# Kernel optimization log

Measured on AMD Instinct MI355X. Metric: run time of the kernel, lower is better.

## Reference

```python
import jax, jax.numpy as jnp
import numpy as np

NUM_HEADS = 16
NEG_INF = -1e18


def setup_inputs() -> dict:
    key = jax.random.key(0)
    ks = jax.random.split(key, 9)
    T, B, D = 2048, 2, 1024
    s = 1.0 / np.sqrt(D)
    return {
        "query": jax.random.normal(ks[0], (T, B, D), jnp.float32),
        "q_w": jax.random.normal(ks[1], (D, D), jnp.float32) * s,
        "q_b": jax.random.normal(ks[2], (D,), jnp.float32) * 0.02,
        "k_w": jax.random.normal(ks[3], (D, D), jnp.float32) * s,
        "k_b": jax.random.normal(ks[4], (D,), jnp.float32) * 0.02,
        "v_w": jax.random.normal(ks[5], (D, D), jnp.float32) * s,
        "v_b": jax.random.normal(ks[6], (D,), jnp.float32) * 0.02,
        "out_w": jax.random.normal(ks[7], (D, D), jnp.float32) * s,
        "out_b": jax.random.normal(ks[8], (D,), jnp.float32) * 0.02,
    }


def reference(query, q_w, q_b, k_w, k_b, v_w, v_b, out_w, out_b):
    # query: [T, B, D] (Time x Batch x Channel). Self-attention, causal mask,
    # dropout=0, need_weights=True.
    T, B, D = query.shape
    H = NUM_HEADS
    hd = D // H
    scaling = 1.0 / jnp.sqrt(jnp.asarray(hd, query.dtype))

    q = (query @ q_w.T + q_b) * scaling
    k = query @ k_w.T + k_b
    v = query @ v_w.T + v_b

    def split_heads(x):  # [T, B, D] -> [B, H, T, hd]
        return x.reshape(T, B, H, hd).transpose(1, 2, 0, 3)

    qh, kh, vh = split_heads(q), split_heads(k), split_heads(v)

    # scores: [B, H, T, T]
    scores = jnp.einsum("bhtd,bhsd->bhts", qh, kh)
    causal = jnp.triu(jnp.full((T, T), NEG_INF, dtype=scores.dtype), k=1)
    scores = scores + causal

    probs = jax.nn.softmax(scores, axis=-1)
    attn = jnp.einsum("bhts,bhsd->bhtd", probs, vh)  # [B, H, T, hd]
    attn = attn.transpose(2, 0, 1, 3).reshape(T, B, D)
    out = attn @ out_w.T + out_b

    # averaged attention weights over heads: [B, T, T]
    avg_weights = probs.sum(axis=1) / H
    return out, avg_weights
```

## Files before the change

kernel.cpp:

```cpp
#include <hip/hip_runtime.h>
#include <hip/hip_bf16.h>
#include <stdint.h>

typedef __hip_bfloat16 bf16;
using short8 = __attribute__((ext_vector_type(8))) short;
using f32x4  = __attribute__((ext_vector_type(4))) float;

#define TDIM 2048
#define BDIM 2
#define DDIM 1024
#define HNUM 16
#define HD   64
#define MDIM 4096
#define M0   16.0f

__device__ __forceinline__ f32x4 mfma16(short8 a, short8 b, f32x4 c) {
  return __builtin_amdgcn_mfma_f32_16x16x32_bf16(a, b, c, 0, 0, 0);
}

union S8 { short8 v; bf16 h[8]; };
union P4 { uint2 u; bf16 h[4]; };

__global__ __launch_bounds__(256) void cast_all_kernel(
    const float* __restrict__ q, const float* __restrict__ wq,
    const float* __restrict__ wk, const float* __restrict__ wv,
    const float* __restrict__ wo, bf16* __restrict__ dst) {
  int t4 = blockIdx.x * blockDim.x + threadIdx.x;
  int idx = t4 * 4;
  const float* s;
  if (idx < 4194304)      s = q  + idx;
  else if (idx < 5242880) s = wq + (idx - 4194304);
  else if (idx < 6291456) s = wk + (idx - 5242880);
  else if (idx < 7340032) s = wv + (idx - 6291456);
  else                    s = wo + (idx - 7340032);
  float4 v = *(const float4*)s;
  union { ushort4 u; bf16 b[4]; } pk;
  pk.b[0] = __float2bfloat16(v.x);
  pk.b[1] = __float2bfloat16(v.y);
  pk.b[2] = __float2bfloat16(v.z);
  pk.b[3] = __float2bfloat16(v.w);
  *(ushort4*)(dst + idx) = pk.u;
}

__global__ __launch_bounds__(256) void qkv_kernel(
    const bf16* __restrict__ X, const bf16* __restrict__ Wq,
    const bf16* __restrict__ Wk, const bf16* __restrict__ Wv,
    const float* __restrict__ qb, const float* __restrict__ kb,
    const float* __restrict__ vb, bf16* __restrict__ Qo,
    bf16* __restrict__ Ko, bf16* __restrict__ Vto) {
  __shared__ __align__(16) bf16 Xs[64][72];
  __shared__ __align__(16) bf16 Qs[64][72];
  __shared__ __align__(16) bf16 Ks[64][72];
  __shared__ __align__(16) bf16 Vs[64][72];
  const int tid  = threadIdx.x;
  const int lane = tid & 63, wave = tid >> 6;
  const int m0 = blockIdx.y * 64, n0 = blockIdx.x * 64;
  const int wm = (wave >> 1) * 32, wn = (wave & 1) * 32;
  const int fr = lane & 15, quad = lane >> 4, q8 = quad * 8;
  const int r = tid >> 3, cc = (tid & 7) * 8;
  f32x4 aq[2][2] = {}, ak[2][2] = {}, av[2][2] = {};
  const bf16* xp0 = X  + (size_t)(m0 + r) * DDIM + cc;
  const bf16* xp1 = xp0 + 32 * DDIM;
  const bf16* qp0 = Wq + (size_t)(n0 + r) * DDIM + cc;
  const bf16* qp1 = qp0 + 32 * DDIM;
  const bf16* kp0 = Wk + (size_t)(n0 + r) * DDIM + cc;
  const bf16* kp1 = kp0 + 32 * DDIM;
  const bf16* vp0 = Wv + (size_t)(n0 + r) * DDIM + cc;
  const bf16* vp1 = vp0 + 32 * DDIM;
  for (int k0 = 0; k0 < DDIM; k0 += 64) {
    uint4 xv0 = *(const uint4*)(xp0 + k0), xv1 = *(const uint4*)(xp1 + k0);
    uint4 qv0 = *(const uint4*)(qp0 + k0), qv1 = *(const uint4*)(qp1 + k0);
    uint4 kv0 = *(const uint4*)(kp0 + k0), kv1 = *(const uint4*)(kp1 + k0);
    uint4 vv0 = *(const uint4*)(vp0 + k0), vv1 = *(const uint4*)(vp1 + k0);
    __syncthreads();
    *(uint4*)&Xs[r][cc] = xv0; *(uint4*)&Xs[r + 32][cc] = xv1;
    *(uint4*)&Qs[r][cc] = qv0; *(uint4*)&Qs[r + 32][cc] = qv1;
    *(uint4*)&Ks[r][cc] = kv0; *(uint4*)&Ks[r + 32][cc] = kv1;
    *(uint4*)&Vs[r][cc] = vv0; *(uint4*)&Vs[r + 32][cc] = vv1;
    __syncthreads();
#pragma unroll
    for (int kk = 0; kk < 2; kk++) {
      const int ko = kk * 32 + q8;
      short8 xf[2], qf[2], kf[2], vf[2];
#pragma unroll
      for (int j = 0; j < 2; j++) {
        xf[j] = *(const short8*)&Xs[wm + j * 16 + fr][ko];
        qf[j] = *(const short8*)&Qs[wn + j * 16 + fr][ko];
        kf[j] = *(const short8*)&Ks[wn + j * 16 + fr][ko];
        vf[j] = *(const short8*)&Vs[wn + j * 16 + fr][ko];
      }
#pragma unroll
      for (int i = 0; i < 2; i++)
#pragma unroll
        for (int j = 0; j < 2; j++) {
          aq[i][j] = mfma16(xf[i], qf[j], aq[i][j]);
          ak[i][j] = mfma16(xf[i], kf[j], ak[i][j]);
          av[i][j] = mfma16(vf[i], xf[j], av[i][j]);
        }
    }
  }
#pragma unroll
  for (int mt = 0; mt < 2; mt++)
#pragma unroll
    for (int nt = 0; nt < 2; nt++)
#pragma unroll
      for (int i = 0; i < 4; i++) {
        {
          int gm = m0 + wm + mt * 16 + quad * 4 + i;
          int gn = n0 + wn + nt * 16 + fr;
          int t = gm >> 1, bb = gm & 1, h = gn >> 6, e = gn & 63;
          size_t o = ((size_t)(bb * HNUM + h) * TDIM + t) * HD + e;
          Qo[o] = __float2bfloat16((aq[mt][nt][i] + qb[gn]) * 0.125f);
          Ko[o] = __float2bfloat16(ak[mt][nt][i] + kb[gn]);
        }
        {
          int gf = n0 + wn + mt * 16 + quad * 4 + i;
          int gt = m0 + wm + nt * 16 + fr;
          int t = gt >> 1, bb = gt & 1, h = gf >> 6, e = gf & 63;
          Vto[((size_t)(bb * HNUM + h) * HD + e) * TDIM + t] =
              __float2bfloat16(av[mt][nt][i] + vb[gf]);
        }
      }
}

__global__ __launch_bounds__(256) void gemm_out_kernel(
    const bf16* __restrict__ P0, const bf16* __restrict__ P1,
    const bf16* __restrict__ Bw, const float* __restrict__ l0buf,
    const float* __restrict__ l1buf, const float* __restrict__ bias,
    float* __restrict__ of32) {
  __shared__ __align__(16) bf16 As[64][40];
  __shared__ __align__(16) bf16 Bs[64][40];
  __shared__ float sInv[64][16];
  const int tid  = threadIdx.x;
  const int lane = tid & 63, wave = tid >> 6;
  const int m0 = blockIdx.y * 64, n0 = blockIdx.x * 64;
  const int wm = (wave >> 1) * 32, wn = (wave & 1) * 32;
  const int fr = lane & 15, quad = lane >> 4, q8 = quad * 8;
  const int ldr = tid >> 2, ldc = (tid & 3) * 8;
#pragma unroll
  for (int e = 0; e < 4; e++) {
    int idx = tid * 4 + e;
    int row = idx >> 4, h = idx & 15;
    int gm = m0 + row, t = gm >> 1, bb = gm & 1;
    size_t li = (size_t)(bb * HNUM + h) * TDIM + t;
    sInv[row][h] = 1.0f / (l0buf[li] + l1buf[li]);
  }
  __syncthreads();
  f32x4 acc[2][2] = {};
  const size_t arow = (size_t)(m0 + ldr) * DDIM + ldc;
  const bf16* bptr = Bw + (size_t)(n0 + ldr) * DDIM + ldc;
  for (int k0 = 0; k0 < DDIM; k0 += 32) {
    S8 a0, a1, apk;
    a0.v = *(const short8*)&P0[arow + k0];
    a1.v = *(const short8*)&P1[arow + k0];
    uint4 bvv = *(const uint4*)(bptr + k0);
    float inv = sInv[ldr][k0 >> 6];
#pragma unroll
    for (int k = 0; k < 8; k++)
      apk.h[k] = __float2bfloat16(
          (__bfloat162float(a0.h[k]) + __bfloat162float(a1.h[k])) * inv);
    __syncthreads();
    *(short8*)&As[ldr][ldc] = apk.v;
    *(uint4*)&Bs[ldr][ldc] = bvv;
    __syncthreads();
    short8 af[2], bfr[2];
    af[0]  = *(const short8*)&As[wm + fr][q8];
    af[1]  = *(const short8*)&As[wm + 16 + fr][q8];
    bfr[0] = *(const short8*)&Bs[wn + fr][q8];
    bfr[1] = *(const short8*)&Bs[wn + 16 + fr][q8];
    acc[0][0] = mfma16(af[0], bfr[0], acc[0][0]);
    acc[0][1] = mfma16(af[0], bfr[1], acc[0][1]);
    acc[1][0] = mfma16(af[1], bfr[0], acc[1][0]);
    acc[1][1] = mfma16(af[1], bfr[1], acc[1][1]);
  }
#pragma unroll
  for (int mt = 0; mt < 2; mt++)
#pragma unroll
    for (int nt = 0; nt < 2; nt++)
#pragma unroll
      for (int i = 0; i < 4; i++) {
        int gm = m0 + wm + mt * 16 + quad * 4 + i;
        int gn = n0 + wn + nt * 16 + fr;
        of32[(size_t)gm * DDIM + gn] = acc[mt][nt][i] + bias[gn];
      }
}

__global__ __launch_bounds__(256) void attn_split_kernel(
    const bf16* __restrict__ Q, const bf16* __restrict__ K,
    const bf16* __restrict__ Vt, bf16* __restrict__ P0o,
    bf16* __restrict__ P1o, float* __restrict__ l0buf,
    float* __restrict__ l1buf) {
  __shared__ __align__(16) bf16 Ks[2][64][40];
  __shared__ __align__(16) bf16 Vs[2][64][40];
  __shared__ __align__(16) bf16 pt[4][32][72];
  const int tid = threadIdx.x, lane = tid & 63, wave = tid >> 6;
  const int bid = blockIdx.x;
  const int part = bid & 1, bh = (bid >> 1) & 31, t128 = 15 - (bid >> 6);
  const int b = bh >> 4, h = bh & 15;
  const int t0 = t128 * 128 + wave * 32;
  const int fr = lane & 15, quad = lane >> 4, q8 = quad * 8;
  const bf16* Qp = Q + ((size_t)bh * TDIM + t0) * HD;
  const bf16* Kp = K + (size_t)bh * TDIM * HD;
  const bf16* Vp = Vt + (size_t)bh * HD * TDIM;
  short8 aq[2][2];
  aq[0][0] = *(const short8*)&Qp[fr * HD + q8];
  aq[0][1] = *(const short8*)&Qp[fr * HD + 32 + q8];
  aq[1][0] = *(const short8*)&Qp[(16 + fr) * HD + q8];
  aq[1][1] = *(const short8*)&Qp[(16 + fr) * HD + 32 + q8];
  const int Cb = 2 * t128 + 2, C0 = t128 + 1;
  const int clo = part ? C0 : 0, chi = part ? Cb : C0;
  const int sr0 = tid >> 3, scc = (tid & 7) * 8, sr1 = sr0 + 32;
  const int ssub = scc >> 5, scol = scc & 31;
  f32x4 oacc[2][4] = {};
  float lsum[2] = {0.f, 0.f};
  uint4 kv0, kv1, vv0, vv1;
  auto ldglob = [&](int c) {
    int s0 = c * 64;
    kv0 = *(const uint4*)&Kp[(size_t)(s0 + sr0) * HD + scc];
    kv1 = *(const uint4*)&Kp[(size_t)(s0 + sr1) * HD + scc];
    vv0 = *(const uint4*)&Vp[(size_t)sr0 * TDIM + s0 + scc];
    vv1 = *(const uint4*)&Vp[(size_t)sr1 * TDIM + s0 + scc];
  };
  ldglob(clo);
  for (int c = clo; c < chi; c++) {
    __syncthreads();
    *(uint4*)&Ks[ssub][sr0][scol] = kv0;
    *(uint4*)&Ks[ssub][sr1][scol] = kv1;
    *(uint4*)&Vs[ssub][sr0][scol] = vv0;
    *(uint4*)&Vs[ssub][sr1][scol] = vv1;
    __syncthreads();
    if (c + 1 < chi) ldglob(c + 1);
    const int s0 = c * 64;
    f32x4 scT[2][4] = {};
#pragma unroll
    for (int j = 0; j < 4; j++) {
      short8 k0f = *(const short8*)&Ks[0][j * 16 + fr][q8];
      short8 k1f = *(const short8*)&Ks[1][j * 16 + fr][q8];
      scT[0][j] = mfma16(k0f, aq[0][0], scT[0][j]);
      scT[0][j] = mfma16(k1f, aq[0][1], scT[0][j]);
      scT[1][j] = mfma16(k0f, aq[1][0], scT[1][j]);
      scT[1][j] = mfma16(k1f, aq[1][1], scT[1][j]);
    }
#pragma unroll
    for (int g = 0; g < 2; g++) {
      const int t_row = t0 + g * 16 + fr;
#pragma unroll
      for (int j = 0; j < 4; j++) {
        const int s_base = s0 + j * 16 + quad * 4;
        P4 pk;
#pragma unroll
        for (int i = 0; i < 4; i++) {
          float p = 0.f;
          if (s_base + i <= t_row) {
            p = __expf(scT[g][j][i] - M0);
            lsum[g] += p;
          }
          pk.h[i] = __float2bfloat16(p);
        }
        *(uint2*)&pt[wave][g * 16 + fr][j * 16 + quad * 4] = pk.u;
      }
    }
#pragma unroll
    for (int c2 = 0; c2 < 2; c2++) {
      short8 ap0 = *(const short8*)&pt[wave][fr][c2 * 32 + q8];
      short8 ap1 = *(const short8*)&pt[wave][16 + fr][c2 * 32 + q8];
#pragma unroll
      for (int nt = 0; nt < 4; nt++) {
        short8 vf = *(const short8*)&Vs[c2][nt * 16 + fr][q8];
        oacc[0][nt] = mfma16(ap0, vf, oacc[0][nt]);
        oacc[1][nt] = mfma16(ap1, vf, oacc[1][nt]);
      }
    }
  }
  float lr[2];
#pragma unroll
  for (int g = 0; g < 2; g++) {
    float l = lsum[g];
    l += __shfl_xor(l, 16);
    l += __shfl_xor(l, 32);
    lr[g] = l;
  }
  bf16*  Op = part ? P1o : P0o;
  float* lb = part ? l1buf : l0buf;
#pragma unroll
  for (int g = 0; g < 2; g++)
#pragma unroll
    for (int nt = 0; nt < 4; nt++)
#pragma unroll
      for (int i = 0; i < 4; i++) {
        int t_row = t0 + g * 16 + quad * 4 + i;
        int col = h * HD + nt * 16 + fr;
        Op[((size_t)t_row * BDIM + b) * DDIM + col] =
            __float2bfloat16(oacc[g][nt][i]);
      }
  if (quad == 0) {
    lb[(size_t)bh * TDIM + t0 + fr]      = lr[0];
    lb[(size_t)bh * TDIM + t0 + 16 + fr] = lr[1];
  }
}

__global__ __launch_bounds__(256) void avg_kernel(
    const bf16* __restrict__ Q, const bf16* __restrict__ K,
    const float* __restrict__ l0buf, const float* __restrict__ l1buf,
    float* __restrict__ avgw) {
  const int tid = threadIdx.x;
  int r = blockIdx.x;
  const int b = (r >= 2048) ? 1 : 0;
  r &= 2047;
  float* avp = avgw + (size_t)b * TDIM * TDIM;
  if (r >= 1056) {
    int r2 = r - 1056;
    int ti = 0;
    while (ti < 31 && (ti + 1) * (62 - ti) <= r2) ti++;
    int si = (2 * ti + 2) + (r2 - ti * (63 - ti));
    int t0b = ti * 64, s0 = si * 32;
#pragma unroll
    for (int k = 0; k < 2; k++) {
      int off = (tid * 2 + k) * 4;
      *(float4*)&avp[(size_t)(t0b + (off >> 5)) * TDIM + s0 + (off & 31)] =
          make_float4(0.f, 0.f, 0.f, 0.f);
    }
    return;
  }
  int ti = 0;
  while ((ti + 1) * (ti + 2) <= r) ti++;
  const int si = r - ti * (ti + 1);
  const int t0b = ti * 64, s0 = si * 32;

  __shared__ __align__(16) bf16 Qs[2][64][40];
  __shared__ __align__(16) bf16 Ks2[2][32][40];
  __shared__ float sinvl[HNUM][64];
#pragma unroll
  for (int k = 0; k < 4; k++) {
    int idx = tid + k * 256;
    size_t li = (size_t)(b * HNUM + (idx >> 6)) * TDIM + t0b + (idx & 63);
    sinvl[idx >> 6][idx & 63] = 1.0f / (l0buf[li] + l1buf[li]);
  }
  const int lane = tid & 63, wave = tid >> 6;
  const int fr = lane & 15, quad = lane >> 4, q8 = quad * 8;
  const int twr = wave * 16;
  const int qr0 = tid >> 3, qcc = (tid & 7) * 8, qr1 = qr0 + 32;
  const int qsub = qcc >> 5, qcol = qcc & 31;
  const bf16* Qb = Q + (size_t)b * HNUM * TDIM * HD;
  const bf16* Kb = K + (size_t)b * HNUM * TDIM * HD;
  uint4 qv0, qv1, kv1;
  auto ldh = [&](int hh) {
    const bf16* Qh = Qb + (size_t)hh * TDIM * HD;
    const bf16* Kh = Kb + (size_t)hh * TDIM * HD;
    qv0 = *(const uint4*)&Qh[(size_t)(t0b + qr0) * HD + qcc];
    qv1 = *(const uint4*)&Qh[(size_t)(t0b + qr1) * HD + qcc];
    kv1 = *(const uint4*)&Kh[(size_t)(s0 + (qr0 & 31)) * HD + qcc];
  };
  ldh(0);
  f32x4 facc[2] = {};
  for (int hh = 0; hh < HNUM; hh++) {
    __syncthreads();
    *(uint4*)&Qs[qsub][qr0][qcol] = qv0;
    *(uint4*)&Qs[qsub][qr1][qcol] = qv1;
    if (qr0 < 32) *(uint4*)&Ks2[qsub][qr0][qcol] = kv1;
    else          *(uint4*)&Ks2[qsub][qr0 - 32][qcol] = kv1;
    __syncthreads();
    if (hh + 1 < HNUM) ldh(hh + 1);
    short8 a0 = *(const short8*)&Qs[0][twr + fr][q8];
    short8 a1 = *(const short8*)&Qs[1][twr + fr][q8];
#pragma unroll
    for (int nt = 0; nt < 2; nt++) {
      short8 b0 = *(const short8*)&Ks2[0][nt * 16 + fr][q8];
      short8 b1 = *(const short8*)&Ks2[1][nt * 16 + fr][q8];
      f32x4 sc = {};
      sc = mfma16(a0, b0, sc);
      sc = mfma16(a1, b1, sc);
#pragma unroll
      for (int i = 0; i < 4; i++) {
        int tr = twr + quad * 4 + i;
        if (s0 + nt * 16 + fr <= t0b + tr)
          facc[nt][i] += __expf(sc[i] - M0) * sinvl[hh][tr];
      }
    }
  }
#pragma unroll
  for (int nt = 0; nt < 2; nt++)
#pragma unroll
    for (int i = 0; i < 4; i++)
      avp[(size_t)(t0b + twr + quad * 4 + i) * TDIM + s0 + nt * 16 + fr] =
          facc[nt][i] * 0.0625f;
}

extern "C" void kernel_launch(void* const* d_in, const int* in_sizes, int n_in,
                              void* d_out, int out_size, void* d_ws, size_t ws_size,
                              hipStream_t stream) {
  const float* q   = (const float*)d_in[0];
  const float* q_w = (const float*)d_in[1];
  const float* q_b = (const float*)d_in[2];
  const float* k_w = (const float*)d_in[3];
  const float* k_b = (const float*)d_in[4];
  const float* v_w = (const float*)d_in[5];
  const float* v_b = (const float*)d_in[6];
  const float* o_w = (const float*)d_in[7];
  const float* o_b = (const float*)d_in[8];
  float* out = (float*)d_out;
  float* avg = out + (size_t)MDIM * DDIM;

  bf16* ws  = (bf16*)d_ws;
  bf16* Xbf = ws;
  bf16* Wq  = ws + 4194304;
  bf16* Wk  = ws + 5242880;
  bf16* Wv  = ws + 6291456;
  bf16* Wo  = ws + 7340032;
  bf16* Qw  = ws + 8388608;
  bf16* Kw  = ws + 12582912;
  bf16* Vt  = ws + 16777216;
  bf16* P1  = ws + 20971520;
  bf16* P0  = ws;
  float* l0 = (float*)(ws + 4194304);
  float* l1 = (float*)(ws + 4325376);

  cast_all_kernel<<<8192, 256, 0, stream>>>(q, q_w, k_w, v_w, o_w, Xbf);
  qkv_kernel<<<dim3(16, 64), 256, 0, stream>>>(Xbf, Wq, Wk, Wv, q_b, k_b, v_b,
                                               Qw, Kw, Vt);
  attn_split_kernel<<<1024, 256, 0, stream>>>(Qw, Kw, Vt, P0, P1, l0, l1);
  avg_kernel<<<4096, 256, 0, stream>>>(Qw, Kw, l0, l1, avg);
  gemm_out_kernel<<<dim3(16, 64), 256, 0, stream>>>(P0, P1, Wo, l0, l1, o_b, out);
}
```

Measured before the change: 252.0 us.

## Enlarge QKV tile to 128 rows and prefetch next k-tile in projection GEMMs

The QKV projection kernel now computes a 128x64 output tile per block instead of 64x64, so each loaded weight tile is reused across twice as many rows and the grid is halved. Both the QKV and output GEMMs now load the next k-slice into registers while the current slice is being multiplied, a register-level software pipeline meant to hide global memory latency. The output GEMM's k-step also grows from 32 to 64 to cut barrier count. The cost is more registers and LDS per block, which may lower occupancy, and fewer blocks in the QKV grid.

```diff
diff --git a/kernel.cpp b/kernel.cpp
--- a/kernel.cpp
+++ b/kernel.cpp
@@ -42,84 +42,99 @@
   *(ushort4*)(dst + idx) = pk.u;
 }
 
-__global__ __launch_bounds__(256) void qkv_kernel(
+__global__ __launch_bounds__(256, 2) void qkv_kernel(
     const bf16* __restrict__ X, const bf16* __restrict__ Wq,
     const bf16* __restrict__ Wk, const bf16* __restrict__ Wv,
     const float* __restrict__ qb, const float* __restrict__ kb,
     const float* __restrict__ vb, bf16* __restrict__ Qo,
     bf16* __restrict__ Ko, bf16* __restrict__ Vto) {
-  __shared__ __align__(16) bf16 Xs[64][72];
+  __shared__ __align__(16) bf16 Xs[128][72];
   __shared__ __align__(16) bf16 Qs[64][72];
   __shared__ __align__(16) bf16 Ks[64][72];
   __shared__ __align__(16) bf16 Vs[64][72];
   const int tid  = threadIdx.x;
   const int lane = tid & 63, wave = tid >> 6;
-  const int m0 = blockIdx.y * 64, n0 = blockIdx.x * 64;
-  const int wm = (wave >> 1) * 32, wn = (wave & 1) * 32;
+  const int m0 = blockIdx.y * 128, n0 = blockIdx.x * 64;
+  const int wm = (wave >> 1) * 64, wn = (wave & 1) * 32;
   const int fr = lane & 15, quad = lane >> 4, q8 = quad * 8;
   const int r = tid >> 3, cc = (tid & 7) * 8;
-  f32x4 aq[2][2] = {}, ak[2][2] = {}, av[2][2] = {};
-  const bf16* xp0 = X  + (size_t)(m0 + r) * DDIM + cc;
-  const bf16* xp1 = xp0 + 32 * DDIM;
-  const bf16* qp0 = Wq + (size_t)(n0 + r) * DDIM + cc;
-  const bf16* qp1 = qp0 + 32 * DDIM;
-  const bf16* kp0 = Wk + (size_t)(n0 + r) * DDIM + cc;
-  const bf16* kp1 = kp0 + 32 * DDIM;
-  const bf16* vp0 = Wv + (size_t)(n0 + r) * DDIM + cc;
-  const bf16* vp1 = vp0 + 32 * DDIM;
+  f32x4 aq[4][2] = {}, ak[4][2] = {}, av[2][4] = {};
+  const bf16* xp = X  + (size_t)(m0 + r) * DDIM + cc;
+  const bf16* qp = Wq + (size_t)(n0 + r) * DDIM + cc;
+  const bf16* kp = Wk + (size_t)(n0 + r) * DDIM + cc;
+  const bf16* vp = Wv + (size_t)(n0 + r) * DDIM + cc;
+  uint4 xv[4], qv[2], kv[2], vv[2];
+  auto ld = [&](int k0) {
+#pragma unroll
+    for (int j = 0; j < 4; j++)
+      xv[j] = *(const uint4*)(xp + (size_t)j * 32 * DDIM + k0);
+#pragma unroll
+    for (int j = 0; j < 2; j++) {
+      qv[j] = *(const uint4*)(qp + (size_t)j * 32 * DDIM + k0);
+      kv[j] = *(const uint4*)(kp + (size_t)j * 32 * DDIM + k0);
+      vv[j] = *(const uint4*)(vp + (size_t)j * 32 * DDIM + k0);
+    }
+  };
+  ld(0);
   for (int k0 = 0; k0 < DDIM; k0 += 64) {
-    uint4 xv0 = *(const uint4*)(xp0 + k0), xv1 = *(const uint4*)(xp1 + k0);
-    uint4 qv0 = *(const uint4*)(qp0 + k0), qv1 = *(const uint4*)(qp1 + k0);
-    uint4 kv0 = *(const uint4*)(kp0 + k0), kv1 = *(const uint4*)(kp1 + k0);
-    uint4 vv0 = *(const uint4*)(vp0 + k0), vv1 = *(const uint4*)(vp1 + k0);
-    __syncthreads();
-    *(uint4*)&Xs[r][cc] = xv0; *(uint4*)&Xs[r + 32][cc] = xv1;
-    *(uint4*)&Qs[r][cc] = qv0; *(uint4*)&Qs[r + 32][cc] = qv1;
-    *(uint4*)&Ks[r][cc] = kv0; *(uint4*)&Ks[r + 32][cc] = kv1;
-    *(uint4*)&Vs[r][cc] = vv0; *(uint4*)&Vs[r + 32][cc] = vv1;
-    __syncthreads();
+    __syncthreads();
+#pragma unroll
+    for (int j = 0; j < 4; j++) *(uint4*)&Xs[r + j * 32][cc] = xv[j];
+#pragma unroll
+    for (int j = 0; j < 2; j++) {
+      *(uint4*)&Qs[r + j * 32][cc] = qv[j];
+      *(uint4*)&Ks[r + j * 32][cc] = kv[j];
+      *(uint4*)&Vs[r + j * 32][cc] = vv[j];
+    }
+    __syncthreads();
+    if (k0 + 64 < DDIM) ld(k0 + 64);
 #pragma unroll
     for (int kk = 0; kk < 2; kk++) {
       const int ko = kk * 32 + q8;
-      short8 xf[2], qf[2], kf[2], vf[2];
+      short8 xf[4], qf[2], kf[2], vf[2];
+#pragma unroll
+      for (int i = 0; i < 4; i++)
+        xf[i] = *(const short8*)&Xs[wm + i * 16 + fr][ko];
 #pragma unroll
       for (int j = 0; j < 2; j++) {
-        xf[j] = *(const short8*)&Xs[wm + j * 16 + fr][ko];
         qf[j] = *(const short8*)&Qs[wn + j * 16 + fr][ko];
         kf[j] = *(const short8*)&Ks[wn + j * 16 + fr][ko];
         vf[j] = *(const short8*)&Vs[wn + j * 16 + fr][ko];
       }
 #pragma unroll
-      for (int i = 0; i < 2; i++)
+      for (int i = 0; i < 4; i++)
 #pragma unroll
         for (int j = 0; j < 2; j++) {
           aq[i][j] = mfma16(xf[i], qf[j], aq[i][j]);
           ak[i][j] = mfma16(xf[i], kf[j], ak[i][j]);
-          av[i][j] = mfma16(vf[i], xf[j], av[i][j]);
+          av[j][i] = mfma16(vf[j], xf[i], av[j][i]);
         }
     }
   }
 #pragma unroll
-  for (int mt = 0; mt < 2; mt++)
+  for (int mt = 0; mt < 4; mt++)
 #pragma unroll
     for (int nt = 0; nt < 2; nt++)
 #pragma unroll
       for (int i = 0; i < 4; i++) {
-        {
-          int gm = m0 + wm + mt * 16 + quad * 4 + i;
-          int gn = n0 + wn + nt * 16 + fr;
-          int t = gm >> 1, bb = gm & 1, h = gn >> 6, e = gn & 63;
-          size_t o = ((size_t)(bb * HNUM + h) * TDIM + t) * HD + e;
-          Qo[o] = __float2bfloat16((aq[mt][nt][i] + qb[gn]) * 0.125f);
-          Ko[o] = __float2bfloat16(ak[mt][nt][i] + kb[gn]);
-        }
-        {
-          int gf = n0 + wn + mt * 16 + quad * 4 + i;
-          int gt = m0 + wm + nt * 16 + fr;
-          int t = gt >> 1, bb = gt & 1, h = gf >> 6, e = gf & 63;
-          Vto[((size_t)(bb * HNUM + h) * HD + e) * TDIM + t] =
-              __float2bfloat16(av[mt][nt][i] + vb[gf]);
-        }
+        int gm = m0 + wm + mt * 16 + quad * 4 + i;
+        int gn = n0 + wn + nt * 16 + fr;
+        int t = gm >> 1, bb = gm & 1, h = gn >> 6, e = gn & 63;
+        size_t o = ((size_t)(bb * HNUM + h) * TDIM + t) * HD + e;
+        Qo[o] = __float2bfloat16((aq[mt][nt][i] + qb[gn]) * 0.125f);
+        Ko[o] = __float2bfloat16(ak[mt][nt][i] + kb[gn]);
+      }
+#pragma unroll
+  for (int vt = 0; vt < 2; vt++)
+#pragma unroll
+    for (int xt = 0; xt < 4; xt++)
+#pragma unroll
+      for (int i = 0; i < 4; i++) {
+        int gf = n0 + wn + vt * 16 + quad * 4 + i;
+        int gt = m0 + wm + xt * 16 + fr;
+        int t = gt >> 1, bb = gt & 1, h = gf >> 6, e = gf & 63;
+        Vto[((size_t)(bb * HNUM + h) * HD + e) * TDIM + t] =
+            __float2bfloat16(av[vt][xt][i] + vb[gf]);
       }
 }
 
@@ -128,15 +143,15 @@
     const bf16* __restrict__ Bw, const float* __restrict__ l0buf,
     const float* __restrict__ l1buf, const float* __restrict__ bias,
     float* __restrict__ of32) {
-  __shared__ __align__(16) bf16 As[64][40];
-  __shared__ __align__(16) bf16 Bs[64][40];
+  __shared__ __align__(16) bf16 As[64][72];
+  __shared__ __align__(16) bf16 Bs[64][72];
   __shared__ float sInv[64][16];
   const int tid  = threadIdx.x;
   const int lane = tid & 63, wave = tid >> 6;
   const int m0 = blockIdx.y * 64, n0 = blockIdx.x * 64;
   const int wm = (wave >> 1) * 32, wn = (wave & 1) * 32;
   const int fr = lane & 15, quad = lane >> 4, q8 = quad * 8;
-  const int ldr = tid >> 2, ldc = (tid & 3) * 8;
+  const int ldr = tid >> 3, ldc = (tid & 7) * 8;
 #pragma unroll
   for (int e = 0; e < 4; e++) {
     int idx = tid * 4 + e;
@@ -145,33 +160,54 @@
     size_t li = (size_t)(bb * HNUM + h) * TDIM + t;
     sInv[row][h] = 1.0f / (l0buf[li] + l1buf[li]);
   }
+  f32x4 acc[2][2] = {};
+  const size_t ar0 = (size_t)(m0 + ldr) * DDIM + ldc;
+  const size_t ar1 = ar0 + (size_t)32 * DDIM;
+  const bf16* bp0 = Bw + (size_t)(n0 + ldr) * DDIM + ldc;
+  const bf16* bp1 = bp0 + (size_t)32 * DDIM;
+  S8 p00, p10, p01, p11;
+  uint4 bv0, bv1;
+  auto ld = [&](int k0) {
+    p00.v = *(const short8*)&P0[ar0 + k0];
+    p10.v = *(const short8*)&P1[ar0 + k0];
+    p01.v = *(const short8*)&P0[ar1 + k0];
+    p11.v = *(const short8*)&P1[ar1 + k0];
+    bv0 = *(const uint4*)(bp0 + k0);
+    bv1 = *(const uint4*)(bp1 + k0);
+  };
+  ld(0);
   __syncthreads();
-  f32x4 acc[2][2] = {};
-  const size_t arow = (size_t)(m0 + ldr) * DDIM + ldc;
-  const bf16* bptr = Bw + (size_t)(n0 + ldr) * DDIM + ldc;
-  for (int k0 = 0; k0 < DDIM; k0 += 32) {
-    S8 a0, a1, apk;
-    a0.v = *(const short8*)&P0[arow + k0];
-    a1.v = *(const short8*)&P1[arow + k0];
-    uint4 bvv = *(const uint4*)(bptr + k0);
-    float inv = sInv[ldr][k0 >> 6];
-#pragma unroll
-    for (int k = 0; k < 8; k++)
-      apk.h[k] = __float2bfloat16(
-          (__bfloat162float(a0.h[k]) + __bfloat162float(a1.h[k])) * inv);
-    __syncthreads();
-    *(short8*)&As[ldr][ldc] = apk.v;
-    *(uint4*)&Bs[ldr][ldc] = bvv;
-    __syncthreads();
-    short8 af[2], bfr[2];
-    af[0]  = *(const short8*)&As[wm + fr][q8];
-    af[1]  = *(const short8*)&As[wm + 16 + fr][q8];
-    bfr[0] = *(const short8*)&Bs[wn + fr][q8];
-    bfr[1] = *(const short8*)&Bs[wn + 16 + fr][q8];
-    acc[0][0] = mfma16(af[0], bfr[0], acc[0][0]);
-    acc[0][1] = mfma16(af[0], bfr[1], acc[0][1]);
-    acc[1][0] = mfma16(af[1], bfr[0], acc[1][0]);
-    acc[1][1] = mfma16(af[1], bfr[1], acc[1][1]);
+  for (int k0 = 0; k0 < DDIM; k0 += 64) {
+    const float inv0 = sInv[ldr][k0 >> 6];
+    const float inv1 = sInv[ldr + 32][k0 >> 6];
+    S8 w0, w1;
+#pragma unroll
+    for (int k = 0; k < 8; k++) {
+      w0.h[k] = __float2bfloat16(
+          (__bfloat162float(p00.h[k]) + __bfloat162float(p10.h[k])) * inv0);
+      w1.h[k] = __float2bfloat16(
+          (__bfloat162float(p01.h[k]) + __bfloat162float(p11.h[k])) * inv1);
+    }
+    __syncthreads();
+    *(short8*)&As[ldr][ldc]      = w0.v;
+    *(short8*)&As[ldr + 32][ldc] = w1.v;
+    *(uint4*)&Bs[ldr][ldc]       = bv0;
+    *(uint4*)&Bs[ldr + 32][ldc]  = bv1;
+    __syncthreads();
+    if (k0 + 64 < DDIM) ld(k0 + 64);
+#pragma unroll
+    for (int kk = 0; kk < 2; kk++) {
+      const int ko = kk * 32 + q8;
+      short8 af[2], bfr[2];
+      af[0]  = *(const short8*)&As[wm + fr][ko];
+      af[1]  = *(const short8*)&As[wm + 16 + fr][ko];
+      bfr[0] = *(const short8*)&Bs[wn + fr][ko];
+      bfr[1] = *(const short8*)&Bs[wn + 16 + fr][ko];
+      acc[0][0] = mfma16(af[0], bfr[0], acc[0][0]);
+      acc[0][1] = mfma16(af[0], bfr[1], acc[0][1]);
+      acc[1][0] = mfma16(af[1], bfr[0], acc[1][0]);
+      acc[1][1] = mfma16(af[1], bfr[1], acc[1][1]);
+    }
   }
 #pragma unroll
   for (int mt = 0; mt < 2; mt++)
@@ -416,7 +452,7 @@
   float* l1 = (float*)(ws + 4325376);
 
   cast_all_kernel<<<8192, 256, 0, stream>>>(q, q_w, k_w, v_w, o_w, Xbf);
-  qkv_kernel<<<dim3(16, 64), 256, 0, stream>>>(Xbf, Wq, Wk, Wv, q_b, k_b, v_b,
+  qkv_kernel<<<dim3(16, 32), 256, 0, stream>>>(Xbf, Wq, Wk, Wv, q_b, k_b, v_b,
                                                Qw, Kw, Vt);
   attn_split_kernel<<<1024, 256, 0, stream>>>(Qw, Kw, Vt, P0, P1, l0, l1);
   avg_kernel<<<4096, 256, 0, stream>>>(Qw, Kw, l0, l1, avg);
```

New measurement: 311.3 us. 1.24x slower.
